# Kernel optimization log

Measured on AMD Instinct MI355X. Metric: run time of the kernel, lower is better.

The kernel has to match this reference:

```python
import jax, jax.numpy as jnp
import numpy as np

DIM = 512
HEADS = 16
GRID = (32, 32)
MLP_HIDDEN = 2048
EPS = 1e-5


def _relative_position_index(hw):
    H, W = hw
    coords = np.stack(np.meshgrid(np.arange(H), np.arange(W), indexing='ij'))  # [2,H,W]
    coords = coords.reshape(2, -1)  # [2, L]
    rel = coords[:, :, None] - coords[:, None, :]  # [2, L, L]
    rel = rel.transpose(1, 2, 0).astype(np.int64)  # [L, L, 2]
    rel[:, :, 0] += H - 1
    rel[:, :, 1] += W - 1
    rel[:, :, 0] *= 2 * W - 1
    return jnp.asarray(rel.sum(-1))  # [L, L]


def setup_inputs() -> dict:
    key = jax.random.key(0)
    ks = jax.random.split(key, 12)
    L = GRID[0] * GRID[1]
    table_size = (2 * GRID[0] - 1) * (2 * GRID[1] - 1)
    s = 0.02
    return {
        'x': jax.random.normal(ks[0], (8, L, DIM), jnp.float32),
        'rel_index': _relative_position_index(GRID),
        'bias_table': s * jax.random.truncated_normal(ks[1], -2.0, 2.0, (table_size, HEADS), jnp.float32),
        'qkv_w': jax.random.normal(ks[2], (DIM, 3 * DIM), jnp.float32) / np.sqrt(DIM),
        'qkv_b': jnp.zeros((3 * DIM,), jnp.float32),
        'proj_w': jax.random.normal(ks[3], (DIM, DIM), jnp.float32) / np.sqrt(DIM),
        'proj_b': jnp.zeros((DIM,), jnp.float32),
        'n1_g': jnp.ones((DIM,), jnp.float32),
        'n1_b': jnp.zeros((DIM,), jnp.float32),
        'n2_g': jnp.ones((DIM,), jnp.float32),
        'n2_b': jnp.zeros((DIM,), jnp.float32),
        'fc1_w': jax.random.normal(ks[4], (DIM, MLP_HIDDEN), jnp.float32) / np.sqrt(DIM),
        'fc1_b': jnp.zeros((MLP_HIDDEN,), jnp.float32),
        'fc2_w': jax.random.normal(ks[5], (MLP_HIDDEN, DIM), jnp.float32) / np.sqrt(MLP_HIDDEN),
        'fc2_b': jnp.zeros((DIM,), jnp.float32),
    }


def _layernorm(x, g, b):
    mu = jnp.mean(x, -1, keepdims=True)
    var = jnp.mean(jnp.square(x - mu), -1, keepdims=True)
    return (x - mu) * jax.lax.rsqrt(var + EPS) * g + b


def reference(x, rel_index, bias_table, qkv_w, qkv_b, proj_w, proj_b,
              n1_g, n1_b, n2_g, n2_b, fc1_w, fc1_b, fc2_w, fc2_b):
    B, L, C = x.shape
    hd = C // HEADS
    scale = hd ** -0.5

    h = _layernorm(x, n1_g, n1_b)
    qkv = (h @ qkv_w + qkv_b).reshape(B, L, 3, HEADS, hd)
    qkv = jnp.transpose(qkv, (2, 0, 3, 1, 4))  # [3, B, H, L, hd]
    q, k, v = qkv[0] * scale, qkv[1], qkv[2]

    attn = jnp.einsum('bhld,bhmd->bhlm', q, k)  # [B, H, L, L]
    bias = bias_table[rel_index]                # [L, L, H]
    attn = attn + jnp.transpose(bias, (2, 0, 1))[None]
    attn = jax.nn.softmax(attn, axis=-1)

    out = jnp.einsum('bhlm,bhmd->bhld', attn, v)
    out = jnp.transpose(out, (0, 2, 1, 3)).reshape(B, L, C)
    out = out @ proj_w + proj_b

    x = x + out
    h2 = _layernorm(x, n2_g, n2_b)
    mlp = jax.nn.gelu(h2 @ fc1_w + fc1_b, approximate=False) @ fc2_w + fc2_b
    return x + mlp
```

## Files before the change

### kernel.cpp

```cpp
#include <hip/hip_runtime.h>

typedef unsigned short u16;
typedef __attribute__((ext_vector_type(8))) short bf16x8;
typedef __attribute__((ext_vector_type(4))) float f32x4;

__device__ __forceinline__ float bf2f(unsigned int u) {
    union { unsigned int i; float f; } c; c.i = u << 16; return c.f;
}
__device__ __forceinline__ unsigned int f2bf(float f) {
    union { float f; unsigned int i; } c; c.f = f;
    unsigned int x = c.i;
    unsigned int r = x + 0x7FFFu + ((x >> 16) & 1u);
    return r >> 16;
}

__device__ __forceinline__ void gload_lds16(const u16* g, u16* l) {
    __builtin_amdgcn_global_load_lds(
        (__attribute__((address_space(1))) void*)const_cast<u16*>(g),
        (__attribute__((address_space(3))) void*)l,
        16, 0, 0);
}

__global__ __launch_bounds__(256) void wconv_kernel(const float* __restrict__ W,
                                                    u16* __restrict__ Wt, int K, int N) {
    __shared__ u16 tile[32][36];
    int k0 = blockIdx.y * 32, n0 = blockIdx.x * 32;
    int t = threadIdx.x;
    int r = t >> 3, c4 = (t & 7) * 4;
    float4 v = *(const float4*)(W + (size_t)(k0 + r) * N + n0 + c4);
    tile[r][c4 + 0] = (u16)f2bf(v.x);
    tile[r][c4 + 1] = (u16)f2bf(v.y);
    tile[r][c4 + 2] = (u16)f2bf(v.z);
    tile[r][c4 + 3] = (u16)f2bf(v.w);
    __syncthreads();
    int n = t >> 3, k4 = (t & 7) * 4;
    u16 a0 = tile[k4 + 0][n], a1 = tile[k4 + 1][n];
    u16 a2 = tile[k4 + 2][n], a3 = tile[k4 + 3][n];
    uint2 st;
    st.x = (unsigned)a0 | ((unsigned)a1 << 16);
    st.y = (unsigned)a2 | ((unsigned)a3 << 16);
    *(uint2*)(Wt + (size_t)(n0 + n) * K + k0 + k4) = st;
}

__global__ __launch_bounds__(256) void ln_kernel(const float* __restrict__ x,
                                                 const float* __restrict__ g,
                                                 const float* __restrict__ b,
                                                 u16* __restrict__ y) {
    int row = blockIdx.x * 4 + (threadIdx.x >> 6);
    int t = threadIdx.x & 63;
    const float* xr = x + (size_t)row * 512 + t * 8;
    float4 a = *(const float4*)xr;
    float4 c = *(const float4*)(xr + 4);
    float v[8] = { a.x, a.y, a.z, a.w, c.x, c.y, c.z, c.w };
    float s = 0.f, ss = 0.f;
#pragma unroll
    for (int i = 0; i < 8; ++i) { s += v[i]; ss += v[i] * v[i]; }
#pragma unroll
    for (int off = 32; off; off >>= 1) {
        s  += __shfl_down(s, off);
        ss += __shfl_down(ss, off);
    }
    s = __shfl(s, 0); ss = __shfl(ss, 0);
    float mu = s * (1.0f / 512.0f);
    float var = ss * (1.0f / 512.0f) - mu * mu;
    float r = rsqrtf(var + 1e-5f);
    float4 g0 = *(const float4*)(g + t * 8);
    float4 g1 = *(const float4*)(g + t * 8 + 4);
    float4 b0 = *(const float4*)(b + t * 8);
    float4 b1 = *(const float4*)(b + t * 8 + 4);
    float gv[8] = { g0.x, g0.y, g0.z, g0.w, g1.x, g1.y, g1.z, g1.w };
    float bv[8] = { b0.x, b0.y, b0.z, b0.w, b1.x, b1.y, b1.z, b1.w };
    unsigned int o[4];
#pragma unroll
    for (int i = 0; i < 4; ++i) {
        float o0 = (v[2 * i] - mu) * r * gv[2 * i] + bv[2 * i];
        float o1 = (v[2 * i + 1] - mu) * r * gv[2 * i + 1] + bv[2 * i + 1];
        o[i] = f2bf(o0) | (f2bf(o1) << 16);
    }
    *(uint4*)(y + (size_t)row * 512 + t * 8) = make_uint4(o[0], o[1], o[2], o[3]);
}

template <int ACT, int RES, int COUT>
__global__ __launch_bounds__(256) void gemm_mfma(const u16* __restrict__ A, int lda,
                                                 const u16* __restrict__ Bt,
                                                 const float* __restrict__ bias,
                                                 const float* __restrict__ res, int ldres,
                                                 void* __restrict__ C, int ldC, int K) {
    __shared__ u16 As[64 * 32];
    __shared__ u16 Bs[128 * 32];
    int tid = threadIdx.x;
    int bm = blockIdx.y * 64, bn = blockIdx.x * 128;
    int lane = tid & 63, wv = tid >> 6;
    int q = lane >> 4, lr = lane & 15;
    int wr = wv >> 1, wc = wv & 1;

    const u16* Ag = A + (size_t)(bm + wv * 16 + (lane >> 2)) * lda + (lane & 3) * 8;
    const u16* Bg = Bt + (size_t)(bn + wv * 32 + (lane >> 2)) * K + (lane & 3) * 8;
    u16* Al0 = &As[(wv * 16) * 32];
    u16* Bl0 = &Bs[(wv * 32) * 32];
    u16* Bl1 = &Bs[(wv * 32 + 16) * 32];

    const u16* Apf = &As[(wr * 32 + lr) * 32 + q * 8];
    const u16* Bpf = &Bs[(wc * 64 + lr) * 32 + q * 8];

    f32x4 acc[2][4];
#pragma unroll
    for (int i = 0; i < 2; ++i)
#pragma unroll
        for (int j = 0; j < 4; ++j) acc[i][j] = (f32x4){0.f, 0.f, 0.f, 0.f};

    for (int k0 = 0; k0 < K; k0 += 32) {
        __syncthreads();
        gload_lds16(Ag + k0, Al0);
        gload_lds16(Bg + k0, Bl0);
        gload_lds16(Bg + (size_t)16 * K + k0, Bl1);
        __syncthreads();
        bf16x8 af[2], bfr[4];
#pragma unroll
        for (int i = 0; i < 2; ++i) af[i] = *(const bf16x8*)(Apf + i * 16 * 32);
#pragma unroll
        for (int j = 0; j < 4; ++j) bfr[j] = *(const bf16x8*)(Bpf + j * 16 * 32);
#pragma unroll
        for (int i = 0; i < 2; ++i)
#pragma unroll
            for (int j = 0; j < 4; ++j)
                acc[i][j] = __builtin_amdgcn_mfma_f32_16x16x32_bf16(af[i], bfr[j], acc[i][j], 0, 0, 0);
    }

    float bv[4];
#pragma unroll
    for (int j = 0; j < 4; ++j)
        bv[j] = bias ? bias[bn + wc * 64 + j * 16 + lr] : 0.f;
#pragma unroll
    for (int i = 0; i < 2; ++i) {
#pragma unroll
        for (int j = 0; j < 4; ++j) {
            int col = bn + wc * 64 + j * 16 + lr;
#pragma unroll
            for (int r = 0; r < 4; ++r) {
                int row = bm + wr * 32 + i * 16 + q * 4 + r;
                float v = acc[i][j][r] + bv[j];
                if (ACT) v = 0.5f * v * (1.0f + erff(v * 0.7071067811865475f));
                if (RES) v += res[(size_t)row * ldres + col];
                if (COUT == 0) ((u16*)C)[(size_t)row * ldC + col] = (u16)f2bf(v);
                else           ((float*)C)[(size_t)row * ldC + col] = v;
            }
        }
    }
}

__global__ __launch_bounds__(256) void attn_mfma(u16* __restrict__ qkv,
                                                 const float* __restrict__ bias_table) {
    __shared__ u16 Ks[128][40];
    __shared__ u16 Vt[32][136];
    __shared__ u16 Ps[4][16][136];
    __shared__ float biasc[3969];
    int tid = threadIdx.x;
    int qt = blockIdx.x, h = blockIdx.y, z = blockIdx.z;
    u16* qkvz = qkv + (size_t)z * 1024 * 1536;

    const float LOG2E = 1.4426950408889634f;
    for (int i = tid; i < 3969; i += 256) biasc[i] = bias_table[(size_t)i * 16 + h] * LOG2E;

    int lane = tid & 63, wv = tid >> 6;
    int q = lane >> 4, m = lane & 15;

    int qrow = qt * 64 + wv * 16 + m;
    bf16x8 qf;
    {
        const float qs = 0.17677669529663687f * LOG2E;
        bf16x8 qraw = *(const bf16x8*)(qkvz + (size_t)qrow * 1536 + h * 32 + q * 8);
#pragma unroll
        for (int j = 0; j < 8; ++j)
            qf[j] = (short)f2bf(bf2f((unsigned short)qraw[j]) * qs);
    }

    int arow[4];
#pragma unroll
    for (int r = 0; r < 4; ++r) {
        int l = qt * 64 + wv * 16 + q * 4 + r;
        arow[r] = (l >> 5) * 63 + (l & 31) + 1984;
    }

    float mrow[4] = { -1e30f, -1e30f, -1e30f, -1e30f };
    f32x4 acco[3] = { (f32x4){0.f,0.f,0.f,0.f}, (f32x4){0.f,0.f,0.f,0.f},
                      (f32x4){0.f,0.f,0.f,0.f} };
    bf16x8 onesv;
#pragma unroll
    for (int j = 0; j < 8; ++j) onesv[j] = (short)0x3F80;

    int key = tid >> 1, dh = (tid & 1) * 16;
    const u16* kvsrc = qkvz + (size_t)key * 1536 + 512 + h * 32 + dh;
    uint4 pk0, pk1, pv0, pv1;
    pk0 = *(const uint4*)(kvsrc);
    pk1 = *(const uint4*)(kvsrc + 8);
    pv0 = *(const uint4*)(kvsrc + 512);
    pv1 = *(const uint4*)(kvsrc + 520);

    for (int kt = 0; kt < 8; ++kt) {
        __syncthreads();
        *(uint4*)&Ks[key][dh] = pk0;
        *(uint4*)&Ks[key][dh + 8] = pk1;
        {
            u16 tmp[16];
            *(uint4*)tmp = pv0; *(uint4*)(tmp + 8) = pv1;
#pragma unroll
            for (int j = 0; j < 16; ++j) Vt[dh + j][key] = tmp[j];
        }
        __syncthreads();
        if (kt < 7) {
            const u16* src = kvsrc + (size_t)(kt + 1) * 128 * 1536;
            pk0 = *(const uint4*)(src);
            pk1 = *(const uint4*)(src + 8);
            pv0 = *(const uint4*)(src + 512);
            pv1 = *(const uint4*)(src + 520);
        }

        f32x4 s8[8];
#pragma unroll
        for (int t = 0; t < 8; ++t) {
            bf16x8 kf = *(const bf16x8*)&Ks[t * 16 + m][q * 8];
            s8[t] = __builtin_amdgcn_mfma_f32_16x16x32_bf16(
                qf, kf, (f32x4){0.f,0.f,0.f,0.f}, 0, 0, 0);
        }
#pragma unroll
        for (int t = 0; t < 8; ++t) {
            int bb = (kt * 4 + (t >> 1)) * 63 + (t & 1) * 16 + m;
#pragma unroll
            for (int r = 0; r < 4; ++r)
                s8[t][r] += biasc[arow[r] - bb];
        }
        float alpha[4];
#pragma unroll
        for (int r = 0; r < 4; ++r) {
            float v = s8[0][r];
#pragma unroll
            for (int t = 1; t < 8; ++t) v = fmaxf(v, s8[t][r]);
            v = fmaxf(v, __shfl_xor(v, 1));
            v = fmaxf(v, __shfl_xor(v, 2));
            v = fmaxf(v, __shfl_xor(v, 4));
            v = fmaxf(v, __shfl_xor(v, 8));
            float mn = fmaxf(mrow[r], v);
            alpha[r] = exp2f(mrow[r] - mn);
            mrow[r] = mn;
#pragma unroll
            for (int t = 0; t < 8; ++t)
                s8[t][r] = exp2f(s8[t][r] - mn);
        }
#pragma unroll
        for (int t = 0; t < 8; ++t)
#pragma unroll
            for (int r = 0; r < 4; ++r)
                Ps[wv][q * 4 + r][t * 16 + m] = (u16)f2bf(s8[t][r]);
#pragma unroll
        for (int dt = 0; dt < 3; ++dt)
#pragma unroll
            for (int r = 0; r < 4; ++r) acco[dt][r] *= alpha[r];
#pragma unroll
        for (int c = 0; c < 4; ++c) {
            bf16x8 pf = *(const bf16x8*)&Ps[wv][m][c * 32 + q * 8];
#pragma unroll
            for (int dt = 0; dt < 2; ++dt) {
                bf16x8 vf = *(const bf16x8*)&Vt[dt * 16 + m][c * 32 + q * 8];
                acco[dt] = __builtin_amdgcn_mfma_f32_16x16x32_bf16(pf, vf, acco[dt], 0, 0, 0);
            }
            acco[2] = __builtin_amdgcn_mfma_f32_16x16x32_bf16(pf, onesv, acco[2], 0, 0, 0);
        }
    }
#pragma unroll
    for (int r = 0; r < 4; ++r) {
        int l = qt * 64 + wv * 16 + q * 4 + r;
        float inv = 1.0f / acco[2][r];
#pragma unroll
        for (int dt = 0; dt < 2; ++dt)
            qkvz[(size_t)l * 1536 + h * 32 + dt * 16 + m] = (u16)f2bf(acco[dt][r] * inv);
    }
}

extern "C" void kernel_launch(void* const* d_in, const int* in_sizes, int n_in,
                              void* d_out, int out_size, void* d_ws, size_t ws_size,
                              hipStream_t stream) {
    const float* x          = (const float*)d_in[0];
    const float* bias_table = (const float*)d_in[2];
    const float* qkv_w      = (const float*)d_in[3];
    const float* qkv_b      = (const float*)d_in[4];
    const float* proj_w     = (const float*)d_in[5];
    const float* proj_b     = (const float*)d_in[6];
    const float* n1g        = (const float*)d_in[7];
    const float* n1b        = (const float*)d_in[8];
    const float* n2g        = (const float*)d_in[9];
    const float* n2b        = (const float*)d_in[10];
    const float* fc1_w      = (const float*)d_in[11];
    const float* fc1_b      = (const float*)d_in[12];
    const float* fc2_w      = (const float*)d_in[13];
    const float* fc2_b      = (const float*)d_in[14];
    float* out = (float*)d_out;

    u16* ws16 = (u16*)d_ws;
    u16* wq_t = ws16;
    u16* wp_t = ws16 + 786432;
    u16* w1_t = ws16 + 1048576;
    u16* w2_t = ws16 + 2097152;
    u16* h    = ws16 + 3145728;
    u16* qkvb = ws16 + 7340032;
    u16* hid  = qkvb;

    wconv_kernel<<<dim3(48, 16), 256, 0, stream>>>(qkv_w, wq_t, 512, 1536);
    wconv_kernel<<<dim3(16, 16), 256, 0, stream>>>(proj_w, wp_t, 512, 512);
    wconv_kernel<<<dim3(64, 16), 256, 0, stream>>>(fc1_w, w1_t, 512, 2048);
    wconv_kernel<<<dim3(16, 64), 256, 0, stream>>>(fc2_w, w2_t, 2048, 512);

    ln_kernel<<<2048, 256, 0, stream>>>(x, n1g, n1b, h);

    for (int half = 0; half < 2; ++half) {
        size_t ro = (size_t)half * 4096;
        gemm_mfma<0, 0, 0><<<dim3(12, 64), 256, 0, stream>>>(
            h + ro * 512, 512, wq_t, qkv_b, nullptr, 0, qkvb, 1536, 512);
        attn_mfma<<<dim3(16, 16, 4), 256, 0, stream>>>(qkvb, bias_table);
        gemm_mfma<0, 1, 1><<<dim3(4, 64), 256, 0, stream>>>(
            qkvb, 1536, wp_t, proj_b, x + ro * 512, 512, out + ro * 512, 512, 512);
    }

    ln_kernel<<<2048, 256, 0, stream>>>(out, n2g, n2b, h);

    for (int half = 0; half < 2; ++half) {
        size_t ro = (size_t)half * 4096;
        gemm_mfma<1, 0, 0><<<dim3(16, 64), 256, 0, stream>>>(
            h + ro * 512, 512, w1_t, fc1_b, nullptr, 0, hid, 2048, 512);
        gemm_mfma<0, 1, 1><<<dim3(4, 64), 256, 0, stream>>>(
            hid, 2048, w2_t, fc2_b, out + ro * 512, 512, out + ro * 512, 512, 2048);
    }
}
```

Measured before the change: 395.2 us.

## Double-buffer GEMM LDS tiles, pack V transpose stores, store bias in bf16

```diff
diff --git a/kernel.cpp b/kernel.cpp
--- a/kernel.cpp
+++ b/kernel.cpp
@@ -86,8 +86,8 @@
                                                  const float* __restrict__ bias,
                                                  const float* __restrict__ res, int ldres,
                                                  void* __restrict__ C, int ldC, int K) {
-    __shared__ u16 As[64 * 32];
-    __shared__ u16 Bs[128 * 32];
+    __shared__ u16 As[2][64 * 32];
+    __shared__ u16 Bs[2][128 * 32];
     int tid = threadIdx.x;
     int bm = blockIdx.y * 64, bn = blockIdx.x * 128;
     int lane = tid & 63, wv = tid >> 6;
@@ -96,12 +96,11 @@
 
     const u16* Ag = A + (size_t)(bm + wv * 16 + (lane >> 2)) * lda + (lane & 3) * 8;
     const u16* Bg = Bt + (size_t)(bn + wv * 32 + (lane >> 2)) * K + (lane & 3) * 8;
-    u16* Al0 = &As[(wv * 16) * 32];
-    u16* Bl0 = &Bs[(wv * 32) * 32];
-    u16* Bl1 = &Bs[(wv * 32 + 16) * 32];
-
-    const u16* Apf = &As[(wr * 32 + lr) * 32 + q * 8];
-    const u16* Bpf = &Bs[(wc * 64 + lr) * 32 + q * 8];
+    int aoff  = (wv * 16) * 32;
+    int boff0 = (wv * 32) * 32;
+    int boff1 = (wv * 32 + 16) * 32;
+    int apf = (wr * 32 + lr) * 32 + q * 8;
+    int bpf = (wc * 64 + lr) * 32 + q * 8;
 
     f32x4 acc[2][4];
 #pragma unroll
@@ -109,22 +108,31 @@
 #pragma unroll
         for (int j = 0; j < 4; ++j) acc[i][j] = (f32x4){0.f, 0.f, 0.f, 0.f};
 
+    gload_lds16(Ag, &As[0][aoff]);
+    gload_lds16(Bg, &Bs[0][boff0]);
+    gload_lds16(Bg + (size_t)16 * K, &Bs[0][boff1]);
+    __syncthreads();
+
+    int cur = 0;
     for (int k0 = 0; k0 < K; k0 += 32) {
-        __syncthreads();
-        gload_lds16(Ag + k0, Al0);
-        gload_lds16(Bg + k0, Bl0);
-        gload_lds16(Bg + (size_t)16 * K + k0, Bl1);
-        __syncthreads();
+        int nxt = cur ^ 1;
+        if (k0 + 32 < K) {
+            gload_lds16(Ag + k0 + 32, &As[nxt][aoff]);
+            gload_lds16(Bg + k0 + 32, &Bs[nxt][boff0]);
+            gload_lds16(Bg + (size_t)16 * K + k0 + 32, &Bs[nxt][boff1]);
+        }
         bf16x8 af[2], bfr[4];
 #pragma unroll
-        for (int i = 0; i < 2; ++i) af[i] = *(const bf16x8*)(Apf + i * 16 * 32);
-#pragma unroll
-        for (int j = 0; j < 4; ++j) bfr[j] = *(const bf16x8*)(Bpf + j * 16 * 32);
+        for (int i = 0; i < 2; ++i) af[i] = *(const bf16x8*)&As[cur][apf + i * 16 * 32];
+#pragma unroll
+        for (int j = 0; j < 4; ++j) bfr[j] = *(const bf16x8*)&Bs[cur][bpf + j * 16 * 32];
 #pragma unroll
         for (int i = 0; i < 2; ++i)
 #pragma unroll
             for (int j = 0; j < 4; ++j)
                 acc[i][j] = __builtin_amdgcn_mfma_f32_16x16x32_bf16(af[i], bfr[j], acc[i][j], 0, 0, 0);
+        __syncthreads();
+        cur = nxt;
     }
 
     float bv[4];
@@ -154,13 +162,14 @@
     __shared__ u16 Ks[128][40];
     __shared__ u16 Vt[32][136];
     __shared__ u16 Ps[4][16][136];
-    __shared__ float biasc[3969];
+    __shared__ u16 biasc[3969];
     int tid = threadIdx.x;
     int qt = blockIdx.x, h = blockIdx.y, z = blockIdx.z;
     u16* qkvz = qkv + (size_t)z * 1024 * 1536;
 
     const float LOG2E = 1.4426950408889634f;
-    for (int i = tid; i < 3969; i += 256) biasc[i] = bias_table[(size_t)i * 16 + h] * LOG2E;
+    for (int i = tid; i < 3969; i += 256)
+        biasc[i] = (u16)f2bf(bias_table[(size_t)i * 16 + h] * LOG2E);
 
     int lane = tid & 63, wv = tid >> 6;
     int q = lane >> 4, m = lane & 15;
@@ -190,30 +199,34 @@
     for (int j = 0; j < 8; ++j) onesv[j] = (short)0x3F80;
 
     int key = tid >> 1, dh = (tid & 1) * 16;
-    const u16* kvsrc = qkvz + (size_t)key * 1536 + 512 + h * 32 + dh;
+    int pr = tid & 63, g = tid >> 6;
+    const u16* ksrc0 = qkvz + (size_t)key * 1536 + 512 + h * 32 + dh;
+    const u16* vsrc0 = qkvz + (size_t)(2 * pr) * 1536 + 1024 + h * 32 + g * 8;
     uint4 pk0, pk1, pv0, pv1;
-    pk0 = *(const uint4*)(kvsrc);
-    pk1 = *(const uint4*)(kvsrc + 8);
-    pv0 = *(const uint4*)(kvsrc + 512);
-    pv1 = *(const uint4*)(kvsrc + 520);
+    pk0 = *(const uint4*)(ksrc0);
+    pk1 = *(const uint4*)(ksrc0 + 8);
+    pv0 = *(const uint4*)(vsrc0);
+    pv1 = *(const uint4*)(vsrc0 + 1536);
 
     for (int kt = 0; kt < 8; ++kt) {
         __syncthreads();
         *(uint4*)&Ks[key][dh] = pk0;
         *(uint4*)&Ks[key][dh + 8] = pk1;
         {
-            u16 tmp[16];
-            *(uint4*)tmp = pv0; *(uint4*)(tmp + 8) = pv1;
-#pragma unroll
-            for (int j = 0; j < 16; ++j) Vt[dh + j][key] = tmp[j];
+            u16 a[8], b[8];
+            *(uint4*)a = pv0; *(uint4*)b = pv1;
+#pragma unroll
+            for (int j = 0; j < 8; ++j)
+                *(unsigned int*)&Vt[g * 8 + j][2 * pr] =
+                    (unsigned)a[j] | ((unsigned)b[j] << 16);
         }
         __syncthreads();
         if (kt < 7) {
-            const u16* src = kvsrc + (size_t)(kt + 1) * 128 * 1536;
-            pk0 = *(const uint4*)(src);
-            pk1 = *(const uint4*)(src + 8);
-            pv0 = *(const uint4*)(src + 512);
-            pv1 = *(const uint4*)(src + 520);
+            size_t off = (size_t)(kt + 1) * 128 * 1536;
+            pk0 = *(const uint4*)(ksrc0 + off);
+            pk1 = *(const uint4*)(ksrc0 + off + 8);
+            pv0 = *(const uint4*)(vsrc0 + off);
+            pv1 = *(const uint4*)(vsrc0 + off + 1536);
         }
 
         f32x4 s8[8];
@@ -228,7 +241,7 @@
             int bb = (kt * 4 + (t >> 1)) * 63 + (t & 1) * 16 + m;
 #pragma unroll
             for (int r = 0; r < 4; ++r)
-                s8[t][r] += biasc[arow[r] - bb];
+                s8[t][r] += bf2f(biasc[arow[r] - bb]);
         }
         float alpha[4];
 #pragma unroll
```

Measured after the change: 424.9 us. 1.08x slower.
